# Optimization experiments

Hardware: AMD Instinct MI355X
Metric: run time of the kernel (lower is better)

## Reference

```python
import jax, jax.numpy as jnp
import numpy as np

N, DIM, M, K = 65536, 512, 4, 256
T = 0.9  # gumbel-softmax temperature


def setup_inputs() -> dict:
    key = jax.random.key(0)
    k1, k2, k3, k4 = jax.random.split(key, 4)
    return {
        "x": jax.random.normal(k1, (N, DIM), dtype=jnp.float32),
        "codebooks": jax.random.normal(k2, (M, K, DIM), dtype=jnp.float32) * 0.05,
        "W_att": jax.random.normal(k3, (M, DIM, DIM), dtype=jnp.float32) * 0.05,
        "W_rnn": jax.random.normal(k4, (DIM, DIM), dtype=jnp.float32) * 0.05,
    }


def _gumbel_softmax(logits, temp, hard, key):
    g = jax.random.gumbel(key, logits.shape, logits.dtype)
    y = jax.nn.softmax((logits + g) / temp, axis=-1)
    if hard:
        y_hard = jax.nn.one_hot(jnp.argmax(y, axis=-1), logits.shape[-1], dtype=logits.dtype)
        y = jax.lax.stop_gradient(y_hard - y) + y  # straight-through
    return y


def reference(x, codebooks, W_att, W_rnn):
    noise_key = jax.random.key(42)
    out_sum = jnp.zeros_like(x)
    prev_out = None
    indexes = []
    for i in range(M):  # small fixed number of sequential codebook stages
        if i > 0:  # rnn_mode == 'res'
            x = x - prev_out @ W_rnn
        # bilinear attention: (x W) (C W)^T  -> [N, K]
        x_proj = x @ W_att[i]
        c_proj = codebooks[i] @ W_att[i]
        att_logit = jnp.einsum('nd,kd->nk', x_proj, c_proj)
        k_soft, k_hard = jax.random.split(jax.random.fold_in(noise_key, i))
        weight_soft = _gumbel_softmax(att_logit, T, False, k_soft)
        weight_hard = _gumbel_softmax(att_logit, T, True, k_hard)
        weight = jax.lax.stop_gradient(weight_hard - weight_soft) + weight_soft
        prev_out = weight @ codebooks[i]  # [N, DIM]
        out_sum = out_sum + prev_out
        indexes.append(jnp.argmax(att_logit, axis=-1))
    return out_sum, jnp.stack(indexes, axis=-1)  # [N, DIM], [N, M]
```

## Files before the change

### kernel.cpp

```cpp
#include <hip/hip_runtime.h>
#include <cstdint>
#include <cstddef>
#include <math.h>

#define NROWS 65536
#define DIM   512
#define KCB   256
#define RPW   8
#define RPB   32
#define THR   256
#define LGS   260

__host__ __device__ __forceinline__ uint32_t tf_rotl(uint32_t x, uint32_t r) {
  return (x << r) | (x >> (32u - r));
}
__host__ __device__ inline void tf2x32(uint32_t k0, uint32_t k1,
                                       uint32_t x0, uint32_t x1,
                                       uint32_t& o0, uint32_t& o1) {
  uint32_t k2 = k0 ^ k1 ^ 0x1BD11BDAu;
  x0 += k0; x1 += k1;
#define TF_R(r) { x0 += x1; x1 = tf_rotl(x1, r); x1 ^= x0; }
  TF_R(13) TF_R(15) TF_R(26) TF_R(6)
  x0 += k1; x1 += k2 + 1u;
  TF_R(17) TF_R(29) TF_R(16) TF_R(24)
  x0 += k2; x1 += k0 + 2u;
  TF_R(13) TF_R(15) TF_R(26) TF_R(6)
  x0 += k0; x1 += k1 + 3u;
  TF_R(17) TF_R(29) TF_R(16) TF_R(24)
  x0 += k1; x1 += k2 + 4u;
  TF_R(13) TF_R(15) TF_R(26) TF_R(6)
  x0 += k2; x1 += k0 + 5u;
#undef TF_R
  o0 = x0; o1 = x1;
}

__device__ __forceinline__ float gumbel32(uint32_t k0, uint32_t k1, uint32_t j) {
  uint32_t o0, o1;
  tf2x32(k0, k1, 0u, j, o0, o1);
  uint32_t bits = o0 ^ o1;
  float f = __uint_as_float((bits >> 9) | 0x3f800000u) - 1.0f;
  if (f == 0.0f) f = 1.17549435e-38f;
  float t1 = (float)log((double)f);
  float t2 = (float)log((double)(-t1));
  return -t2;
}

__device__ __forceinline__ float exp32cr(float z) {
  return (float)exp((double)z);
}

__device__ __forceinline__ void argmax64(float& v, int& i) {
#pragma unroll
  for (int off = 32; off >= 1; off >>= 1) {
    float ov = __shfl_xor(v, off);
    int   oi = __shfl_xor(i, off);
    if (ov > v || (ov == v && oi < i)) { v = ov; i = oi; }
  }
}

__device__ __forceinline__ float rdlane(float v, int lane) {
  return __int_as_float(__builtin_amdgcn_readlane(__float_as_int(v), lane));
}

__global__ __launch_bounds__(256) void k_cproj(const float* __restrict__ C,
                                               const float* __restrict__ A,
                                               float* __restrict__ cpd) {
  const int i = blockIdx.x >> 6;
  const int d0 = (blockIdx.x & 63) * 8;
  const int t = threadIdx.x;
  const float* Ai = A + (size_t)i * DIM * DIM;
  const float* Ci = C + (size_t)i * KCB * DIM;
  float acc[8] = {};
  for (int e = 0; e < DIM; ++e) {
    float cv = Ci[(size_t)t * DIM + e];
#pragma unroll
    for (int dd = 0; dd < 8; ++dd)
      acc[dd] = fmaf(cv, Ai[(size_t)e * DIM + d0 + dd], acc[dd]);
  }
#pragma unroll
  for (int dd = 0; dd < 8; ++dd)
    cpd[((size_t)i * DIM + d0 + dd) * KCB + t] = acc[dd];
}

__global__ __launch_bounds__(THR, 3) void k_stage(
    const float* __restrict__ Xin,
    float* __restrict__ Xout,
    const float* __restrict__ Ai,
    const float* __restrict__ cpdi,
    const float* __restrict__ Cbi,
    const float* __restrict__ Wr,
    float* __restrict__ out,
    uint32_t kh0, uint32_t kh1, uint32_t ks0, uint32_t ks1, int stage) {
  __shared__ __align__(16) float lgss[RPB * LGS];
  __shared__ int selL[RPB]; __shared__ int idxL[RPB]; __shared__ float wsL[RPB];
  const int t = threadIdx.x;
  const int L = t & 63;
  const int rb = (t >> 6) * RPW;
  const int n0 = blockIdx.x * RPB;

  float xr[RPW][8];
#pragma unroll
  for (int r = 0; r < RPW; ++r) {
    const float* px = Xin + (size_t)(n0 + rb + r) * 512 + L * 8;
    float4 a = *(const float4*)px;
    float4 b = *(const float4*)(px + 4);
    xr[r][0] = a.x; xr[r][1] = a.y; xr[r][2] = a.z; xr[r][3] = a.w;
    xr[r][4] = b.x; xr[r][5] = b.y; xr[r][6] = b.z; xr[r][7] = b.w;
  }

  float xp[RPW][8];
#pragma unroll
  for (int r = 0; r < RPW; ++r)
#pragma unroll
    for (int c = 0; c < 8; ++c) xp[r][c] = 0.0f;
  for (int eb = 0; eb < 64; ++eb) {
#pragma unroll
    for (int j = 0; j < 8; ++j) {
      const int e = eb * 8 + j;
      const float* arow = Ai + (size_t)e * 512 + L * 8;
      float4 a0 = *(const float4*)arow;
      float4 a1 = *(const float4*)(arow + 4);
      float av[8] = {a0.x, a0.y, a0.z, a0.w, a1.x, a1.y, a1.z, a1.w};
      float xs[RPW];
#pragma unroll
      for (int r = 0; r < RPW; ++r) xs[r] = rdlane(xr[r][j], eb);
#pragma unroll
      for (int r = 0; r < RPW; ++r)
#pragma unroll
        for (int c = 0; c < 8; ++c)
          xp[r][c] = fmaf(xs[r], av[c], xp[r][c]);
    }
  }

  float lacc[RPW][4];
#pragma unroll
  for (int r = 0; r < RPW; ++r)
#pragma unroll
    for (int s = 0; s < 4; ++s) lacc[r][s] = 0.0f;
  for (int db = 0; db < 64; ++db) {
#pragma unroll
    for (int j = 0; j < 8; ++j) {
      const int d = db * 8 + j;
      float4 cv = *(const float4*)(cpdi + (size_t)d * 256 + 4 * L);
      float xs[RPW];
#pragma unroll
      for (int r = 0; r < RPW; ++r) xs[r] = rdlane(xp[r][j], db);
#pragma unroll
      for (int r = 0; r < RPW; ++r) {
        lacc[r][0] = __fadd_rn(lacc[r][0], __fmul_rn(xs[r], cv.x));
        lacc[r][1] = __fadd_rn(lacc[r][1], __fmul_rn(xs[r], cv.y));
        lacc[r][2] = __fadd_rn(lacc[r][2], __fmul_rn(xs[r], cv.z));
        lacc[r][3] = __fadd_rn(lacc[r][3], __fmul_rn(xs[r], cv.w));
      }
    }
  }
#pragma unroll
  for (int r = 0; r < RPW; ++r)
    *(float4*)&lgss[(rb + r) * LGS + 4 * L] =
        make_float4(lacc[r][0], lacc[r][1], lacc[r][2], lacc[r][3]);
  __syncthreads();

  {
    const int c = t & 63;
#pragma unroll 1
    for (int rr2 = 0; rr2 < RPW; ++rr2) {
      const int r = (t >> 6) * RPW + rr2;
      const int n = n0 + r;
      const uint32_t jb = (uint32_t)n * 256u;
      float l[4];
#pragma unroll
      for (int sub = 0; sub < 4; ++sub) l[sub] = lgss[r * LGS + sub * 64 + c];
      float bv = l[0]; int bi = c;
#pragma unroll
      for (int sub = 1; sub < 4; ++sub)
        if (l[sub] > bv) { bv = l[sub]; bi = sub * 64 + c; }
      argmax64(bv, bi);
      float sv = 0.0f; int si = 0;
#pragma unroll
      for (int sub = 0; sub < 4; ++sub) {
        float g = gumbel32(kh0, kh1, jb + (uint32_t)(sub * 64 + c));
        float s = __fdiv_rn(__fadd_rn(l[sub], g), 0.9f);
        if (sub == 0 || s > sv) { sv = s; si = sub * 64 + c; }
      }
      argmax64(sv, si);
      float ssv[4];
#pragma unroll
      for (int sub = 0; sub < 4; ++sub) {
        float g = gumbel32(ks0, ks1, jb + (uint32_t)(sub * 64 + c));
        ssv[sub] = __fdiv_rn(__fadd_rn(l[sub], g), 0.9f);
      }
      float m = fmaxf(fmaxf(ssv[0], ssv[1]), fmaxf(ssv[2], ssv[3]));
#pragma unroll
      for (int off = 32; off >= 1; off >>= 1) m = fmaxf(m, __shfl_xor(m, off));
#pragma unroll
      for (int sub = 0; sub < 4; ++sub)
        lgss[r * LGS + sub * 64 + c] = exp32cr(__fsub_rn(ssv[sub], m));
      if (c == 0) { selL[r] = si; idxL[r] = bi; }
    }
  }
  __syncthreads();

  {
    const int r = t >> 3;
    const int j = t & 7;
    const float* a = lgss + r * LGS;
    float acc0 = a[j];
#pragma unroll
    for (int i = 1; i < 16; ++i) acc0 = __fadd_rn(acc0, a[j + 8 * i]);
    float s0 = __fadd_rn(acc0, __shfl_xor(acc0, 1));
    s0 = __fadd_rn(s0, __shfl_xor(s0, 2));
    s0 = __fadd_rn(s0, __shfl_xor(s0, 4));
    float acc1 = a[128 + j];
#pragma unroll
    for (int i = 1; i < 16; ++i) acc1 = __fadd_rn(acc1, a[128 + j + 8 * i]);
    float s1 = __fadd_rn(acc1, __shfl_xor(acc1, 1));
    s1 = __fadd_rn(s1, __shfl_xor(s1, 2));
    s1 = __fadd_rn(s1, __shfl_xor(s1, 4));
    float S = __fadd_rn(s0, s1);
    if (j == 0) {
      const int n = n0 + r;
      int sel = selL[r];
      float wsv = __fdiv_rn(lgss[r * LGS + sel], S);
      wsL[r] = __fadd_rn(__fsub_rn(1.0f, wsv), wsv);
      out[(size_t)NROWS * DIM + (size_t)n * 4 + stage] = (float)idxL[r];
    }
  }
  __syncthreads();

  float p[RPW][8];
#pragma unroll
  for (int r = 0; r < RPW; ++r) {
    const int n = n0 + rb + r;
    const int sel = selL[rb + r];
    const float wv = wsL[rb + r];
    const float* crow = Cbi + (size_t)sel * 512 + L * 8;
    float4 c0 = *(const float4*)crow;
    float4 c1 = *(const float4*)(crow + 4);
    p[r][0] = __fmul_rn(wv, c0.x); p[r][1] = __fmul_rn(wv, c0.y);
    p[r][2] = __fmul_rn(wv, c0.z); p[r][3] = __fmul_rn(wv, c0.w);
    p[r][4] = __fmul_rn(wv, c1.x); p[r][5] = __fmul_rn(wv, c1.y);
    p[r][6] = __fmul_rn(wv, c1.z); p[r][7] = __fmul_rn(wv, c1.w);
    float* orow = out + (size_t)n * 512 + L * 8;
    if (stage == 0) {
      *(float4*)orow = make_float4(p[r][0], p[r][1], p[r][2], p[r][3]);
      *(float4*)(orow + 4) = make_float4(p[r][4], p[r][5], p[r][6], p[r][7]);
    } else {
      float4 o0 = *(const float4*)orow;
      float4 o1 = *(const float4*)(orow + 4);
      o0.x = __fadd_rn(o0.x, p[r][0]); o0.y = __fadd_rn(o0.y, p[r][1]);
      o0.z = __fadd_rn(o0.z, p[r][2]); o0.w = __fadd_rn(o0.w, p[r][3]);
      o1.x = __fadd_rn(o1.x, p[r][4]); o1.y = __fadd_rn(o1.y, p[r][5]);
      o1.z = __fadd_rn(o1.z, p[r][6]); o1.w = __fadd_rn(o1.w, p[r][7]);
      *(float4*)orow = o0;
      *(float4*)(orow + 4) = o1;
    }
  }

  if (stage < 3) {
    float a2[RPW][8];
#pragma unroll
    for (int r = 0; r < RPW; ++r)
#pragma unroll
      for (int c = 0; c < 8; ++c) a2[r][c] = 0.0f;
    for (int db = 0; db < 64; ++db) {
#pragma unroll
      for (int j = 0; j < 8; ++j) {
        const int d = db * 8 + j;
        const float* wrow = Wr + (size_t)d * 512 + L * 8;
        float4 w0 = *(const float4*)wrow;
        float4 w1 = *(const float4*)(wrow + 4);
        float wv[8] = {w0.x, w0.y, w0.z, w0.w, w1.x, w1.y, w1.z, w1.w};
        float ps[RPW];
#pragma unroll
        for (int r = 0; r < RPW; ++r) ps[r] = rdlane(p[r][j], db);
#pragma unroll
        for (int r = 0; r < RPW; ++r)
#pragma unroll
          for (int c = 0; c < 8; ++c)
            a2[r][c] = fmaf(ps[r], wv[c], a2[r][c]);
      }
    }
#pragma unroll
    for (int r = 0; r < RPW; ++r) {
      const float* px = Xin + (size_t)(n0 + rb + r) * 512 + L * 8;
      float4 x0 = *(const float4*)px;
      float4 x1 = *(const float4*)(px + 4);
      float4 o0, o1;
      o0.x = __fsub_rn(x0.x, a2[r][0]); o0.y = __fsub_rn(x0.y, a2[r][1]);
      o0.z = __fsub_rn(x0.z, a2[r][2]); o0.w = __fsub_rn(x0.w, a2[r][3]);
      o1.x = __fsub_rn(x1.x, a2[r][4]); o1.y = __fsub_rn(x1.y, a2[r][5]);
      o1.z = __fsub_rn(x1.z, a2[r][6]); o1.w = __fsub_rn(x1.w, a2[r][7]);
      float* pxo = Xout + (size_t)(n0 + rb + r) * 512 + L * 8;
      *(float4*)pxo = o0;
      *(float4*)(pxo + 4) = o1;
    }
  }
}

extern "C" void kernel_launch(void* const* d_in, const int* in_sizes, int n_in,
                              void* d_out, int out_size, void* d_ws, size_t ws_size,
                              hipStream_t stream) {
  const float* x  = (const float*)d_in[0];
  const float* Cb = (const float*)d_in[1];
  const float* A  = (const float*)d_in[2];
  const float* Wr = (const float*)d_in[3];
  float* out = (float*)d_out;
  float* ws  = (float*)d_ws;

  float* cpd  = ws;
  float* xcur = ws + 524288;

  uint32_t kh[4][2], ks[4][2];
  for (uint32_t i = 0; i < 4; ++i) {
    uint32_t f0, f1, a0, a1, b0, b1;
    tf2x32(0u, 42u, 0u, i, f0, f1);
    tf2x32(f0, f1, 0u, 0u, a0, a1);
    tf2x32(f0, f1, 0u, 1u, b0, b1);
    ks[i][0] = a0; ks[i][1] = a1;
    kh[i][0] = b0; kh[i][1] = b1;
  }

  k_cproj<<<dim3(256), dim3(256), 0, stream>>>(Cb, A, cpd);

  const int NB = NROWS / RPB;
  for (int i = 0; i < 4; ++i) {
    const float* Xi = (i == 0) ? x : xcur;
    k_stage<<<dim3(NB), dim3(THR), 0, stream>>>(
        Xi, xcur, A + (size_t)i * DIM * DIM, cpd + (size_t)i * DIM * KCB,
        Cb + (size_t)i * KCB * DIM, Wr, out,
        kh[i][0], kh[i][1], ks[i][0], ks[i][1], i);
  }
}
```

Before: 6.191 ms.

## Stage X and P rows through shared memory to cut registers and raise occupancy

The X-projection and W_rnn matmuls no longer keep whole input rows in registers and broadcast them with cross-lane reads. Row halves are now staged into the shared buffer and read back as float2 broadcasts, two weight rows per iteration. Freeing the xr and p register arrays lets launch bounds go from 3 to 4 waves per SIMD, aiming for better latency hiding. The cost is extra LDS traffic and barriers, plus a risk of register spills under the tighter bound.

```diff
diff --git a/kernel.cpp b/kernel.cpp
--- a/kernel.cpp
+++ b/kernel.cpp
@@ -82,7 +82,7 @@
     cpd[((size_t)i * DIM + d0 + dd) * KCB + t] = acc[dd];
 }
 
-__global__ __launch_bounds__(THR, 3) void k_stage(
+__global__ __launch_bounds__(THR, 4) void k_stage(
     const float* __restrict__ Xin,
     float* __restrict__ Xout,
     const float* __restrict__ Ai,
@@ -91,45 +91,51 @@
     const float* __restrict__ Wr,
     float* __restrict__ out,
     uint32_t kh0, uint32_t kh1, uint32_t ks0, uint32_t ks1, int stage) {
-  __shared__ __align__(16) float lgss[RPB * LGS];
+  __shared__ __align__(16) float sh[RPB * LGS];
   __shared__ int selL[RPB]; __shared__ int idxL[RPB]; __shared__ float wsL[RPB];
   const int t = threadIdx.x;
   const int L = t & 63;
   const int rb = (t >> 6) * RPW;
   const int n0 = blockIdx.x * RPB;
 
-  float xr[RPW][8];
-#pragma unroll
-  for (int r = 0; r < RPW; ++r) {
-    const float* px = Xin + (size_t)(n0 + rb + r) * 512 + L * 8;
-    float4 a = *(const float4*)px;
-    float4 b = *(const float4*)(px + 4);
-    xr[r][0] = a.x; xr[r][1] = a.y; xr[r][2] = a.z; xr[r][3] = a.w;
-    xr[r][4] = b.x; xr[r][5] = b.y; xr[r][6] = b.z; xr[r][7] = b.w;
-  }
-
   float xp[RPW][8];
 #pragma unroll
   for (int r = 0; r < RPW; ++r)
 #pragma unroll
     for (int c = 0; c < 8; ++c) xp[r][c] = 0.0f;
-  for (int eb = 0; eb < 64; ++eb) {
-#pragma unroll
-    for (int j = 0; j < 8; ++j) {
-      const int e = eb * 8 + j;
-      const float* arow = Ai + (size_t)e * 512 + L * 8;
-      float4 a0 = *(const float4*)arow;
-      float4 a1 = *(const float4*)(arow + 4);
-      float av[8] = {a0.x, a0.y, a0.z, a0.w, a1.x, a1.y, a1.z, a1.w};
-      float xs[RPW];
-#pragma unroll
-      for (int r = 0; r < RPW; ++r) xs[r] = rdlane(xr[r][j], eb);
+
+#pragma unroll 1
+  for (int h = 0; h < 2; ++h) {
+#pragma unroll
+    for (int q = 0; q < 8; ++q) {
+      const int idx = q * 256 + t;
+      const int row = idx >> 6, c4 = idx & 63;
+      *(float4*)&sh[row * LGS + c4 * 4] =
+          *(const float4*)&Xin[(size_t)(n0 + row) * 512 + h * 256 + c4 * 4];
+    }
+    __syncthreads();
+    for (int eh = 0; eh < 256; eh += 2) {
+      const int e = h * 256 + eh;
+      const float* ar0 = Ai + (size_t)e * 512 + L * 8;
+      float4 a00 = *(const float4*)ar0;
+      float4 a01 = *(const float4*)(ar0 + 4);
+      float4 a10 = *(const float4*)(ar0 + 512);
+      float4 a11 = *(const float4*)(ar0 + 516);
+      float av0[8] = {a00.x, a00.y, a00.z, a00.w, a01.x, a01.y, a01.z, a01.w};
+      float av1[8] = {a10.x, a10.y, a10.z, a10.w, a11.x, a11.y, a11.z, a11.w};
+      float2 xs[RPW];
 #pragma unroll
       for (int r = 0; r < RPW; ++r)
-#pragma unroll
-        for (int c = 0; c < 8; ++c)
-          xp[r][c] = fmaf(xs[r], av[c], xp[r][c]);
-    }
+        xs[r] = *(const float2*)&sh[(rb + r) * LGS + eh];
+#pragma unroll
+      for (int r = 0; r < RPW; ++r) {
+#pragma unroll
+        for (int c = 0; c < 8; ++c) xp[r][c] = fmaf(xs[r].x, av0[c], xp[r][c]);
+#pragma unroll
+        for (int c = 0; c < 8; ++c) xp[r][c] = fmaf(xs[r].y, av1[c], xp[r][c]);
+      }
+    }
+    __syncthreads();
   }
 
   float lacc[RPW][4];
@@ -156,7 +162,7 @@
   }
 #pragma unroll
   for (int r = 0; r < RPW; ++r)
-    *(float4*)&lgss[(rb + r) * LGS + 4 * L] =
+    *(float4*)&sh[(rb + r) * LGS + 4 * L] =
         make_float4(lacc[r][0], lacc[r][1], lacc[r][2], lacc[r][3]);
   __syncthreads();
 
@@ -169,7 +175,7 @@
       const uint32_t jb = (uint32_t)n * 256u;
       float l[4];
 #pragma unroll
-      for (int sub = 0; sub < 4; ++sub) l[sub] = lgss[r * LGS + sub * 64 + c];
+      for (int sub = 0; sub < 4; ++sub) l[sub] = sh[r * LGS + sub * 64 + c];
       float bv = l[0]; int bi = c;
 #pragma unroll
       for (int sub = 1; sub < 4; ++sub)
@@ -194,7 +200,7 @@
       for (int off = 32; off >= 1; off >>= 1) m = fmaxf(m, __shfl_xor(m, off));
 #pragma unroll
       for (int sub = 0; sub < 4; ++sub)
-        lgss[r * LGS + sub * 64 + c] = exp32cr(__fsub_rn(ssv[sub], m));
+        sh[r * LGS + sub * 64 + c] = exp32cr(__fsub_rn(ssv[sub], m));
       if (c == 0) { selL[r] = si; idxL[r] = bi; }
     }
   }
@@ -203,7 +209,7 @@
   {
     const int r = t >> 3;
     const int j = t & 7;
-    const float* a = lgss + r * LGS;
+    const float* a = sh + r * LGS;
     float acc0 = a[j];
 #pragma unroll
     for (int i = 1; i < 16; ++i) acc0 = __fadd_rn(acc0, a[j + 8 * i]);
@@ -220,66 +226,72 @@
     if (j == 0) {
       const int n = n0 + r;
       int sel = selL[r];
-      float wsv = __fdiv_rn(lgss[r * LGS + sel], S);
+      float wsv = __fdiv_rn(sh[r * LGS + sel], S);
       wsL[r] = __fadd_rn(__fsub_rn(1.0f, wsv), wsv);
       out[(size_t)NROWS * DIM + (size_t)n * 4 + stage] = (float)idxL[r];
     }
   }
   __syncthreads();
 
-  float p[RPW][8];
-#pragma unroll
-  for (int r = 0; r < RPW; ++r) {
-    const int n = n0 + rb + r;
-    const int sel = selL[rb + r];
-    const float wv = wsL[rb + r];
-    const float* crow = Cbi + (size_t)sel * 512 + L * 8;
-    float4 c0 = *(const float4*)crow;
-    float4 c1 = *(const float4*)(crow + 4);
-    p[r][0] = __fmul_rn(wv, c0.x); p[r][1] = __fmul_rn(wv, c0.y);
-    p[r][2] = __fmul_rn(wv, c0.z); p[r][3] = __fmul_rn(wv, c0.w);
-    p[r][4] = __fmul_rn(wv, c1.x); p[r][5] = __fmul_rn(wv, c1.y);
-    p[r][6] = __fmul_rn(wv, c1.z); p[r][7] = __fmul_rn(wv, c1.w);
-    float* orow = out + (size_t)n * 512 + L * 8;
-    if (stage == 0) {
-      *(float4*)orow = make_float4(p[r][0], p[r][1], p[r][2], p[r][3]);
-      *(float4*)(orow + 4) = make_float4(p[r][4], p[r][5], p[r][6], p[r][7]);
-    } else {
-      float4 o0 = *(const float4*)orow;
-      float4 o1 = *(const float4*)(orow + 4);
-      o0.x = __fadd_rn(o0.x, p[r][0]); o0.y = __fadd_rn(o0.y, p[r][1]);
-      o0.z = __fadd_rn(o0.z, p[r][2]); o0.w = __fadd_rn(o0.w, p[r][3]);
-      o1.x = __fadd_rn(o1.x, p[r][4]); o1.y = __fadd_rn(o1.y, p[r][5]);
-      o1.z = __fadd_rn(o1.z, p[r][6]); o1.w = __fadd_rn(o1.w, p[r][7]);
-      *(float4*)orow = o0;
-      *(float4*)(orow + 4) = o1;
-    }
-  }
-
+  float a2[RPW][8];
   if (stage < 3) {
-    float a2[RPW][8];
 #pragma unroll
     for (int r = 0; r < RPW; ++r)
 #pragma unroll
       for (int c = 0; c < 8; ++c) a2[r][c] = 0.0f;
-    for (int db = 0; db < 64; ++db) {
-#pragma unroll
-      for (int j = 0; j < 8; ++j) {
-        const int d = db * 8 + j;
-        const float* wrow = Wr + (size_t)d * 512 + L * 8;
-        float4 w0 = *(const float4*)wrow;
-        float4 w1 = *(const float4*)(wrow + 4);
-        float wv[8] = {w0.x, w0.y, w0.z, w0.w, w1.x, w1.y, w1.z, w1.w};
-        float ps[RPW];
-#pragma unroll
-        for (int r = 0; r < RPW; ++r) ps[r] = rdlane(p[r][j], db);
+  }
+#pragma unroll 1
+  for (int h = 0; h < 2; ++h) {
+    float4 p4[RPW];
+#pragma unroll
+    for (int r = 0; r < RPW; ++r) {
+      const int n = n0 + rb + r;
+      const int sel = selL[rb + r];
+      const float wv = wsL[rb + r];
+      float4 cv = *(const float4*)(Cbi + (size_t)sel * 512 + h * 256 + 4 * L);
+      p4[r].x = __fmul_rn(wv, cv.x); p4[r].y = __fmul_rn(wv, cv.y);
+      p4[r].z = __fmul_rn(wv, cv.z); p4[r].w = __fmul_rn(wv, cv.w);
+      float* orow = out + (size_t)n * 512 + h * 256 + 4 * L;
+      if (stage == 0) {
+        *(float4*)orow = p4[r];
+      } else {
+        float4 o = *(const float4*)orow;
+        o.x = __fadd_rn(o.x, p4[r].x); o.y = __fadd_rn(o.y, p4[r].y);
+        o.z = __fadd_rn(o.z, p4[r].z); o.w = __fadd_rn(o.w, p4[r].w);
+        *(float4*)orow = o;
+      }
+    }
+    if (stage < 3) {
+      __syncthreads();
+#pragma unroll
+      for (int r = 0; r < RPW; ++r)
+        *(float4*)&sh[(rb + r) * LGS + 4 * L] = p4[r];
+      __syncthreads();
+      for (int dl = 0; dl < 256; dl += 2) {
+        const int d = h * 256 + dl;
+        const float* wr0 = Wr + (size_t)d * 512 + L * 8;
+        float4 w00 = *(const float4*)wr0;
+        float4 w01 = *(const float4*)(wr0 + 4);
+        float4 w10 = *(const float4*)(wr0 + 512);
+        float4 w11 = *(const float4*)(wr0 + 516);
+        float wv0[8] = {w00.x, w00.y, w00.z, w00.w, w01.x, w01.y, w01.z, w01.w};
+        float wv1[8] = {w10.x, w10.y, w10.z, w10.w, w11.x, w11.y, w11.z, w11.w};
+        float2 ps[RPW];
 #pragma unroll
         for (int r = 0; r < RPW; ++r)
-#pragma unroll
-          for (int c = 0; c < 8; ++c)
-            a2[r][c] = fmaf(ps[r], wv[c], a2[r][c]);
-      }
-    }
+          ps[r] = *(const float2*)&sh[(rb + r) * LGS + dl];
+#pragma unroll
+        for (int r = 0; r < RPW; ++r) {
+#pragma unroll
+          for (int c = 0; c < 8; ++c) a2[r][c] = fmaf(ps[r].x, wv0[c], a2[r][c]);
+#pragma unroll
+          for (int c = 0; c < 8; ++c) a2[r][c] = fmaf(ps[r].y, wv1[c], a2[r][c]);
+        }
+      }
+    }
+  }
+
+  if (stage < 3) {
 #pragma unroll
     for (int r = 0; r < RPW; ++r) {
       const float* px = Xin + (size_t)(n0 + rb + r) * 512 + L * 8;
```

Result: faster. 5.117 ms (-17.3%).
